# Optimization experiments

Hardware: AMD Instinct MI355X
Metric: run time of the kernel (lower is better)

## Reference

```python
import jax, jax.numpy as jnp
import numpy as np

UNITS = 1024
NCLASS = 8000
BATCH = 4096

def setup_inputs() -> dict:
    key = jax.random.key(0)
    k1, k2, k3, k4 = jax.random.split(key, 4)
    inputs = jax.random.randint(k1, (BATCH, 1), 0, NCLASS, dtype=jnp.int32)
    h_tm1 = jax.random.normal(k2, (BATCH, UNITS), dtype=jnp.float32)
    # orthogonal-ish recurrent kernel (scaled normal is fine for a numeric reference)
    recurrent_kernel = jax.random.normal(k3, (UNITS, 4 * UNITS), dtype=jnp.float32) * (1.0 / np.sqrt(UNITS))
    kernel_c = jax.random.normal(k4, (NCLASS, 4 * UNITS), dtype=jnp.float32) * (1.0 / np.sqrt(NCLASS))
    bias_z = jnp.full((UNITS,), 5.0, dtype=jnp.float32)  # initializer=constant(5)
    bias = jnp.zeros((3 * UNITS,), dtype=jnp.float32)
    return {"inputs": inputs, "h_tm1": h_tm1, "recurrent_kernel": recurrent_kernel,
            "kernel_c": kernel_c, "bias_z": bias_z, "bias": bias}

def reference(inputs, h_tm1, recurrent_kernel, kernel_c, bias_z, bias):
    u = h_tm1.shape[-1]
    ch = inputs[:, 0].astype(jnp.int32)
    # one_hot(ch) @ kernel_c == row gather of kernel_c (identical math, O(1) per row)
    c_proj = kernel_c[ch]                      # [B, 4u]
    cz, cr, ch_, co = (c_proj[:, :u], c_proj[:, u:2*u], c_proj[:, 2*u:3*u], c_proj[:, 3*u:])
    Rz, Rr, Rh, Ro = (recurrent_kernel[:, :u], recurrent_kernel[:, u:2*u],
                      recurrent_kernel[:, 2*u:3*u], recurrent_kernel[:, 3*u:])
    z = jax.nn.sigmoid(h_tm1 @ Rz + cz + bias_z)
    r = jax.nn.sigmoid(h_tm1 @ Rr + cr + bias[:u])
    hh = jnp.tanh((r * h_tm1) @ Rh + ch_ + bias[u:2*u])
    h = z * h_tm1 + (1.0 - z) * hh
    o = jnp.tanh(h @ Ro + co + bias[2*u:])
    return (o, h)
```

## Files before the change

kernel.cpp:

```cpp
#include <hip/hip_runtime.h>
#include <stdint.h>

#define UNITS 1024
#define BATCH 4096
#define FOURU 4096

typedef __bf16 bf16x8 __attribute__((ext_vector_type(8)));
typedef float f32x4 __attribute__((ext_vector_type(4)));

__device__ __forceinline__ uint16_t f2bf(float f) {
  uint32_t u = __builtin_bit_cast(uint32_t, f);
  u += 0x7FFFu + ((u >> 16) & 1u);
  return (uint16_t)(u >> 16);
}
__device__ __forceinline__ float bf2f(uint16_t b) {
  uint32_t u = ((uint32_t)b) << 16;
  return __builtin_bit_cast(float, u);
}
__device__ __forceinline__ float fsig(float x) {
  return 1.0f / (1.0f + __expf(-x));
}
__device__ __forceinline__ f32x4 mfma16x16x32(bf16x8 a, bf16x8 b, f32x4 c) {
  return __builtin_amdgcn_mfma_f32_16x16x32_bf16(a, b, c, 0, 0, 0);
}

__device__ __forceinline__ void gll16(uint16_t* lds, const uint16_t* g) {
  __builtin_amdgcn_global_load_lds(
      (const __attribute__((address_space(1))) uint32_t*)g,
      (__attribute__((address_space(3))) uint32_t*)lds, 16, 0, 0);
}

__device__ __forceinline__ int fidx(int row, int l4) {
  return row * 4 + (l4 ^ ((row >> 1) & 3));
}

__device__ __forceinline__ void stage64r(const uint16_t* __restrict__ src,
                                         uint16_t* lds, int tid) {
  const int wb = tid & 192;
  const int row = tid >> 2;
  const int kg = (tid & 3) ^ ((row >> 1) & 3);
  gll16(lds + wb * 8, src + row * UNITS + kg * 8);
}

__global__ __launch_bounds__(256) void prep_kernel(const float* __restrict__ h32,
                                                   uint16_t* __restrict__ hbf,
                                                   const float* __restrict__ R,
                                                   uint16_t* __restrict__ RT) {
  __shared__ float t[32][33];
  const int b = blockIdx.x;
  if (b < 4096) {
    const int i = (b * 256 + threadIdx.x) * 4;
    float4 v = *(const float4*)(h32 + i);
    ushort4 o;
    o.x = f2bf(v.x); o.y = f2bf(v.y); o.z = f2bf(v.z); o.w = f2bf(v.w);
    *(ushort4*)(hbf + i) = o;
  } else {
    const int bb = b - 4096;
    const int n0 = (bb & 127) * 32, k0 = (bb >> 7) * 32;
    const int tx = threadIdx.x & 31, ty = threadIdx.x >> 5;
#pragma unroll
    for (int i = 0; i < 4; ++i)
      t[ty + i * 8][tx] = R[(size_t)(k0 + ty + i * 8) * FOURU + n0 + tx];
    __syncthreads();
#pragma unroll
    for (int i = 0; i < 4; ++i)
      RT[(size_t)(n0 + ty + i * 8) * UNITS + k0 + tx] = f2bf(t[tx][ty + i * 8]);
  }
}

template <int EPI>
__global__ __launch_bounds__(256, 6) void gemm_kernel(
    const uint16_t* __restrict__ abf, const uint16_t* __restrict__ bt,
    const int* __restrict__ idx, const float* __restrict__ kc,
    const float* __restrict__ bz, const float* __restrict__ bias,
    const uint16_t* __restrict__ hbf, const uint16_t* __restrict__ zb_in,
    float* __restrict__ out32, uint16_t* __restrict__ outbf,
    uint16_t* __restrict__ out2bf) {
  __shared__ uint16_t sA[2][64 * 32];
  __shared__ uint16_t sB[2][64 * 32];
  const int tid = threadIdx.x;
  const int lane = tid & 63, wave = tid >> 6;
  const int l15 = lane & 15, l4 = lane >> 4;
  const int fid = blockIdx.y * gridDim.x + blockIdx.x;
  const int qx = (gridDim.x * gridDim.y) >> 3;
  const int nid = (fid & 7) * qx + (fid >> 3);
  const int row0 = (nid & 63) * 64;
  const int col0 = (nid >> 6) * 64;
  const int wr = wave >> 1, wc = wave & 1;
  const uint16_t* pa = abf + (size_t)row0 * UNITS;
  const uint16_t* pb = bt + (size_t)col0 * UNITS;
  f32x4 acc[2][2] = {};

  stage64r(pa, sA[0], tid);
  stage64r(pb, sB[0], tid);
  __syncthreads();

  int cur = 0;
  for (int t = 0; t < 32; ++t) {
    if (t < 31) {
      stage64r(pa + (t + 1) * 32, sA[cur ^ 1], tid);
      stage64r(pb + (t + 1) * 32, sB[cur ^ 1], tid);
    }
    const bf16x8* A8 = (const bf16x8*)sA[cur];
    const bf16x8* B8 = (const bf16x8*)sB[cur];
    bf16x8 af[2], bfr[2];
#pragma unroll
    for (int m = 0; m < 2; ++m) af[m] = A8[fidx(wr * 32 + m * 16 + l15, l4)];
#pragma unroll
    for (int n = 0; n < 2; ++n) bfr[n] = B8[fidx(wc * 32 + n * 16 + l15, l4)];
#pragma unroll
    for (int m = 0; m < 2; ++m)
#pragma unroll
      for (int n = 0; n < 2; ++n)
        acc[m][n] = mfma16x16x32(af[m], bfr[n], acc[m][n]);
    __syncthreads();
    cur ^= 1;
  }

  const bool is_z = (col0 < UNITS);
#pragma unroll
  for (int m = 0; m < 2; ++m) {
#pragma unroll
    for (int q = 0; q < 4; ++q) {
      const int i = row0 + wr * 32 + m * 16 + l4 * 4 + q;
      const int ch = idx[i];
      const float* kcrow = kc + (size_t)ch * FOURU;
#pragma unroll
      for (int n = 0; n < 2; ++n) {
        const int jc = col0 + wc * 32 + n * 16 + l15;
        const float a = acc[m][n][q];
        if (EPI == 0) {
          if (is_z) {
            float z = fsig(a + kcrow[jc] + bz[jc]);
            outbf[(size_t)i * UNITS + jc] = f2bf(z);
          } else {
            const int j = jc - UNITS;
            const size_t ij = (size_t)i * UNITS + j;
            float r = fsig(a + kcrow[jc] + bias[j]);
            out2bf[ij] = f2bf(r * bf2f(hbf[ij]));
          }
        } else if (EPI == 1) {
          const size_t ij = (size_t)i * UNITS + jc;
          float hh = tanhf(a + kcrow[2 * UNITS + jc] + bias[UNITS + jc]);
          float z = bf2f(zb_in[ij]);
          float hv = bf2f(hbf[ij]);
          float hn = z * hv + (1.0f - z) * hh;
          out32[ij] = hn;
          outbf[ij] = f2bf(hn);
        } else {
          const size_t ij = (size_t)i * UNITS + jc;
          out32[ij] = tanhf(a + kcrow[3 * UNITS + jc] + bias[2 * UNITS + jc]);
        }
      }
    }
  }
}

extern "C" void kernel_launch(void* const* d_in, const int* in_sizes, int n_in,
                              void* d_out, int out_size, void* d_ws, size_t ws_size,
                              hipStream_t stream) {
  const int* idx = (const int*)d_in[0];
  const float* h32 = (const float*)d_in[1];
  const float* R = (const float*)d_in[2];
  const float* kc = (const float*)d_in[3];
  const float* bz = (const float*)d_in[4];
  const float* bias = (const float*)d_in[5];

  float* o_out = (float*)d_out;
  float* h_out = o_out + (size_t)BATCH * UNITS;

  uint16_t* hbf = (uint16_t*)d_ws;
  uint16_t* rt = hbf + (size_t)BATCH * UNITS;
  uint16_t* rhb = rt + (size_t)FOURU * UNITS;
  uint16_t* hnb = rhb + (size_t)BATCH * UNITS;
  uint16_t* zbuf = hnb + (size_t)BATCH * UNITS;

  prep_kernel<<<dim3(8192), 256, 0, stream>>>(h32, hbf, R, rt);

  gemm_kernel<0><<<dim3(32, 64), 256, 0, stream>>>(
      hbf, rt, idx, kc, bz, bias, hbf, nullptr, nullptr, zbuf, rhb);

  gemm_kernel<1><<<dim3(16, 64), 256, 0, stream>>>(
      rhb, rt + (size_t)2 * UNITS * UNITS, idx, kc, bz, bias, hbf, zbuf,
      h_out, hnb, nullptr);

  gemm_kernel<2><<<dim3(16, 64), 256, 0, stream>>>(
      hnb, rt + (size_t)3 * UNITS * UNITS, idx, kc, bz, bias, nullptr, nullptr,
      o_out, nullptr, nullptr);
}
```

Before: 110.2 us.

## Overlap R-transpose for Rh/Ro with first GEMM, deepen K tile, prefetch epilogue gathers

The prep kernel now transposes only the z/r half of the recurrent kernel. The Rh/Ro half is transposed by extra workgroups appended to the first GEMM launch, so that conversion overlaps GEMM work instead of running serially before it. The GEMM K-step doubles from 32 to 64, halving the number of barrier iterations, and launch bounds drop from 6 to 4 waves to make room for the larger LDS footprint. Index, kernel_c and bias gathers for the epilogue are issued before the main loop so their latency hides behind the MFMAs, at the cost of extra live registers.

Result: no change. 108.8 us (-1.2%).

```diff
diff --git a/kernel.cpp b/kernel.cpp
--- a/kernel.cpp
+++ b/kernel.cpp
@@ -34,19 +34,38 @@
   return row * 4 + (l4 ^ ((row >> 1) & 3));
 }
 
-__device__ __forceinline__ void stage64r(const uint16_t* __restrict__ src,
+__device__ __forceinline__ void stage64h(const uint16_t* __restrict__ src,
                                          uint16_t* lds, int tid) {
   const int wb = tid & 192;
-  const int row = tid >> 2;
-  const int kg = (tid & 3) ^ ((row >> 1) & 3);
-  gll16(lds + wb * 8, src + row * UNITS + kg * 8);
+#pragma unroll
+  for (int p = 0; p < 2; ++p) {
+    const int gi = p * 256 + tid;
+    const int h = gi >> 8;
+    const int r = (gi >> 2) & 63;
+    const int kg = (gi & 3) ^ ((r >> 1) & 3);
+    gll16(lds + (p * 256 + wb) * 8, src + r * UNITS + h * 32 + kg * 8);
+  }
+}
+
+__device__ __forceinline__ void trans_tile(const float* __restrict__ R,
+                                           uint16_t* __restrict__ RT, int n0,
+                                           int k0, void* smem, int tid) {
+  float(*t)[33] = (float(*)[33])smem;
+  const int tx = tid & 31, ty = tid >> 5;
+#pragma unroll
+  for (int i2 = 0; i2 < 4; ++i2)
+    t[ty + i2 * 8][tx] = R[(size_t)(k0 + ty + i2 * 8) * FOURU + n0 + tx];
+  __syncthreads();
+#pragma unroll
+  for (int i2 = 0; i2 < 4; ++i2)
+    RT[(size_t)(n0 + ty + i2 * 8) * UNITS + k0 + tx] = f2bf(t[tx][ty + i2 * 8]);
 }
 
 __global__ __launch_bounds__(256) void prep_kernel(const float* __restrict__ h32,
                                                    uint16_t* __restrict__ hbf,
                                                    const float* __restrict__ R,
                                                    uint16_t* __restrict__ RT) {
-  __shared__ float t[32][33];
+  __shared__ __align__(16) float t[32][33];
   const int b = blockIdx.x;
   if (b < 4096) {
     const int i = (b * 256 + threadIdx.x) * 4;
@@ -55,93 +74,117 @@
     o.x = f2bf(v.x); o.y = f2bf(v.y); o.z = f2bf(v.z); o.w = f2bf(v.w);
     *(ushort4*)(hbf + i) = o;
   } else {
-    const int bb = b - 4096;
-    const int n0 = (bb & 127) * 32, k0 = (bb >> 7) * 32;
-    const int tx = threadIdx.x & 31, ty = threadIdx.x >> 5;
-#pragma unroll
-    for (int i = 0; i < 4; ++i)
-      t[ty + i * 8][tx] = R[(size_t)(k0 + ty + i * 8) * FOURU + n0 + tx];
-    __syncthreads();
-#pragma unroll
-    for (int i = 0; i < 4; ++i)
-      RT[(size_t)(n0 + ty + i * 8) * UNITS + k0 + tx] = f2bf(t[tx][ty + i * 8]);
+    const int tt = b - 4096;
+    trans_tile(R, RT, (tt & 63) * 32, (tt >> 6) * 32, t, threadIdx.x);
   }
 }
 
 template <int EPI>
-__global__ __launch_bounds__(256, 6) void gemm_kernel(
+__global__ __launch_bounds__(256, 4) void gemm_kernel(
     const uint16_t* __restrict__ abf, const uint16_t* __restrict__ bt,
     const int* __restrict__ idx, const float* __restrict__ kc,
     const float* __restrict__ bz, const float* __restrict__ bias,
     const uint16_t* __restrict__ hbf, const uint16_t* __restrict__ zb_in,
     float* __restrict__ out32, uint16_t* __restrict__ outbf,
-    uint16_t* __restrict__ out2bf) {
-  __shared__ uint16_t sA[2][64 * 32];
-  __shared__ uint16_t sB[2][64 * 32];
+    uint16_t* __restrict__ out2bf, const float* __restrict__ R,
+    uint16_t* __restrict__ rtw) {
+  __shared__ __align__(16) char smem[32 * 1024 + 256];
   const int tid = threadIdx.x;
+  int fid = blockIdx.x;
+
+  if (EPI == 0 && fid >= 2048) {
+    const int tt = fid - 2048;
+    trans_tile(R, rtw, 2048 + (tt & 63) * 32, (tt >> 6) * 32, smem, tid);
+    return;
+  }
+
+  uint16_t* sA = (uint16_t*)smem;
+  uint16_t* sB = (uint16_t*)(smem + 16384);
+  int* sIdx = (int*)(smem + 32 * 1024);
   const int lane = tid & 63, wave = tid >> 6;
   const int l15 = lane & 15, l4 = lane >> 4;
-  const int fid = blockIdx.y * gridDim.x + blockIdx.x;
-  const int qx = (gridDim.x * gridDim.y) >> 3;
-  const int nid = (fid & 7) * qx + (fid >> 3);
+  const int nwg = (EPI == 0) ? 2048 : 1024;
+  const int nid = (fid & 7) * (nwg >> 3) + (fid >> 3);
   const int row0 = (nid & 63) * 64;
   const int col0 = (nid >> 6) * 64;
   const int wr = wave >> 1, wc = wave & 1;
   const uint16_t* pa = abf + (size_t)row0 * UNITS;
   const uint16_t* pb = bt + (size_t)col0 * UNITS;
+  const bool is_z = (EPI != 0) || (col0 < UNITS);
+  const int kcoff = (EPI == 0) ? 0 : (EPI == 1 ? 2 : 3) * UNITS;
   f32x4 acc[2][2] = {};
 
-  stage64r(pa, sA[0], tid);
-  stage64r(pb, sB[0], tid);
+  if (tid < 64) sIdx[tid] = idx[row0 + tid];
+  stage64h(pa, sA, tid);
+  stage64h(pb, sB, tid);
   __syncthreads();
 
+  float kcp[2][4][2], bp[2];
+#pragma unroll
+  for (int n = 0; n < 2; ++n) {
+    const int jc = col0 + wc * 32 + n * 16 + l15;
+    if (EPI == 0)
+      bp[n] = is_z ? bz[jc] : bias[jc - UNITS];
+    else
+      bp[n] = bias[(EPI == 1 ? 1 : 2) * UNITS + jc];
+  }
+#pragma unroll
+  for (int m = 0; m < 2; ++m)
+#pragma unroll
+    for (int q = 0; q < 4; ++q) {
+      const int lr = wr * 32 + m * 16 + l4 * 4 + q;
+      const float* kcrow = kc + (size_t)sIdx[lr] * FOURU + kcoff;
+#pragma unroll
+      for (int n = 0; n < 2; ++n)
+        kcp[m][q][n] = kcrow[col0 + wc * 32 + n * 16 + l15];
+    }
+
   int cur = 0;
-  for (int t = 0; t < 32; ++t) {
-    if (t < 31) {
-      stage64r(pa + (t + 1) * 32, sA[cur ^ 1], tid);
-      stage64r(pb + (t + 1) * 32, sB[cur ^ 1], tid);
-    }
-    const bf16x8* A8 = (const bf16x8*)sA[cur];
-    const bf16x8* B8 = (const bf16x8*)sB[cur];
-    bf16x8 af[2], bfr[2];
-#pragma unroll
-    for (int m = 0; m < 2; ++m) af[m] = A8[fidx(wr * 32 + m * 16 + l15, l4)];
-#pragma unroll
-    for (int n = 0; n < 2; ++n) bfr[n] = B8[fidx(wc * 32 + n * 16 + l15, l4)];
-#pragma unroll
-    for (int m = 0; m < 2; ++m)
+  for (int t = 0; t < 16; ++t) {
+    if (t < 15) {
+      stage64h(pa + (t + 1) * 64, sA + (cur ^ 1) * 4096, tid);
+      stage64h(pb + (t + 1) * 64, sB + (cur ^ 1) * 4096, tid);
+    }
+    const bf16x8* A8 = (const bf16x8*)(sA + cur * 4096);
+    const bf16x8* B8 = (const bf16x8*)(sB + cur * 4096);
+#pragma unroll
+    for (int h = 0; h < 2; ++h) {
+      bf16x8 af[2], bfr[2];
+#pragma unroll
+      for (int m = 0; m < 2; ++m)
+        af[m] = A8[h * 256 + fidx(wr * 32 + m * 16 + l15, l4)];
 #pragma unroll
       for (int n = 0; n < 2; ++n)
-        acc[m][n] = mfma16x16x32(af[m], bfr[n], acc[m][n]);
+        bfr[n] = B8[h * 256 + fidx(wc * 32 + n * 16 + l15, l4)];
+#pragma unroll
+      for (int m = 0; m < 2; ++m)
+#pragma unroll
+        for (int n = 0; n < 2; ++n)
+          acc[m][n] = mfma16x16x32(af[m], bfr[n], acc[m][n]);
+    }
     __syncthreads();
     cur ^= 1;
   }
 
-  const bool is_z = (col0 < UNITS);
 #pragma unroll
   for (int m = 0; m < 2; ++m) {
 #pragma unroll
     for (int q = 0; q < 4; ++q) {
       const int i = row0 + wr * 32 + m * 16 + l4 * 4 + q;
-      const int ch = idx[i];
-      const float* kcrow = kc + (size_t)ch * FOURU;
 #pragma unroll
       for (int n = 0; n < 2; ++n) {
         const int jc = col0 + wc * 32 + n * 16 + l15;
-        const float a = acc[m][n][q];
+        const float a = acc[m][n][q] + kcp[m][q][n] + bp[n];
         if (EPI == 0) {
           if (is_z) {
-            float z = fsig(a + kcrow[jc] + bz[jc]);
-            outbf[(size_t)i * UNITS + jc] = f2bf(z);
+            outbf[(size_t)i * UNITS + jc] = f2bf(fsig(a));
           } else {
-            const int j = jc - UNITS;
-            const size_t ij = (size_t)i * UNITS + j;
-            float r = fsig(a + kcrow[jc] + bias[j]);
-            out2bf[ij] = f2bf(r * bf2f(hbf[ij]));
+            const size_t ij = (size_t)i * UNITS + (jc - UNITS);
+            out2bf[ij] = f2bf(fsig(a) * bf2f(hbf[ij]));
           }
         } else if (EPI == 1) {
           const size_t ij = (size_t)i * UNITS + jc;
-          float hh = tanhf(a + kcrow[2 * UNITS + jc] + bias[UNITS + jc]);
+          float hh = tanhf(a);
           float z = bf2f(zb_in[ij]);
           float hv = bf2f(hbf[ij]);
           float hn = z * hv + (1.0f - z) * hh;
@@ -149,7 +192,7 @@
           outbf[ij] = f2bf(hn);
         } else {
           const size_t ij = (size_t)i * UNITS + jc;
-          out32[ij] = tanhf(a + kcrow[3 * UNITS + jc] + bias[2 * UNITS + jc]);
+          out32[ij] = tanhf(a);
         }
       }
     }
@@ -175,16 +218,16 @@
   uint16_t* hnb = rhb + (size_t)BATCH * UNITS;
   uint16_t* zbuf = hnb + (size_t)BATCH * UNITS;
 
-  prep_kernel<<<dim3(8192), 256, 0, stream>>>(h32, hbf, R, rt);
-
-  gemm_kernel<0><<<dim3(32, 64), 256, 0, stream>>>(
-      hbf, rt, idx, kc, bz, bias, hbf, nullptr, nullptr, zbuf, rhb);
-
-  gemm_kernel<1><<<dim3(16, 64), 256, 0, stream>>>(
+  prep_kernel<<<dim3(6144), 256, 0, stream>>>(h32, hbf, R, rt);
+
+  gemm_kernel<0><<<dim3(4096), 256, 0, stream>>>(
+      hbf, rt, idx, kc, bz, bias, hbf, nullptr, nullptr, zbuf, rhb, R, rt);
+
+  gemm_kernel<1><<<dim3(1024), 256, 0, stream>>>(
       rhb, rt + (size_t)2 * UNITS * UNITS, idx, kc, bz, bias, hbf, zbuf,
-      h_out, hnb, nullptr);
-
-  gemm_kernel<2><<<dim3(16, 64), 256, 0, stream>>>(
+      h_out, hnb, nullptr, nullptr, nullptr);
+
+  gemm_kernel<2><<<dim3(1024), 256, 0, stream>>>(
       hnb, rt + (size_t)3 * UNITS * UNITS, idx, kc, bz, bias, nullptr, nullptr,
-      o_out, nullptr, nullptr);
-}
+      o_out, nullptr, nullptr, nullptr, nullptr);
+}
```
